# Kernel optimization log

Hardware: AMD Instinct MI355X
Metric: run time of the kernel (lower is better)

Reference implementation:

```python
import jax, jax.numpy as jnp
import numpy as np

BOX_WARP = 1.0
RAY_START = 2.25
RAY_END = 3.3
S = 32  # depth_resolution (coarse), N_importance = 0


def bilinear_sample(image, coords):
    """Faithful port of the custom grid_sample (align_corners=True mapping).
    image: [B, C, H, W]; coords: [B, M, 2] in [-1, 1]. Returns [B, M, C]."""
    B, C, H, W = image.shape
    ix = (coords[..., 0] + 1.0) * 0.5 * (W - 1)
    iy = (coords[..., 1] + 1.0) * 0.5 * (H - 1)
    ix0 = jnp.floor(ix)
    iy0 = jnp.floor(iy)
    ix1 = ix0 + 1.0
    iy1 = iy0 + 1.0
    # weights use UNclamped corner positions, matching the torch code
    w_nw = (ix1 - ix) * (iy1 - iy)
    w_ne = (ix - ix0) * (iy1 - iy)
    w_sw = (ix1 - ix) * (iy - iy0)
    w_se = (ix - ix0) * (iy - iy0)
    ix0c = jnp.clip(ix0, 0, W - 1).astype(jnp.int32)
    ix1c = jnp.clip(ix1, 0, W - 1).astype(jnp.int32)
    iy0c = jnp.clip(iy0, 0, H - 1).astype(jnp.int32)
    iy1c = jnp.clip(iy1, 0, H - 1).astype(jnp.int32)
    img = image.reshape(B, C, H * W)

    def gather(iyc, ixc):
        idx = iyc * W + ixc  # [B, M]
        return jnp.take_along_axis(img, idx[:, None, :], axis=2)  # [B, C, M]

    out = (gather(iy0c, ix0c) * w_nw[:, None, :]
           + gather(iy0c, ix1c) * w_ne[:, None, :]
           + gather(iy1c, ix0c) * w_sw[:, None, :]
           + gather(iy1c, ix1c) * w_se[:, None, :])
    return out.transpose(0, 2, 1)  # [B, M, C]


def setup_inputs() -> dict:
    key = jax.random.key(0)
    k1, k2, k3, k4, k5 = jax.random.split(key, 5)
    N, n_planes, C, H, W = 2, 3, 32, 256, 256
    R = 16384
    vol_planes = jax.random.normal(k1, (N, n_planes, C, H, W), dtype=jnp.float32)
    dirs = jax.random.normal(k2, (N, R, 3), dtype=jnp.float32)
    dirs = dirs / jnp.linalg.norm(dirs, axis=-1, keepdims=True)
    # camera on sphere of radius 2.7 looking through origin -> samples in box
    ray_origins = -2.7 * dirs
    w1 = jax.random.normal(k3, (C, 64), dtype=jnp.float32) * (1.0 / np.sqrt(C))
    b1 = jnp.zeros((64,), dtype=jnp.float32)
    w2 = jax.random.normal(k4, (64, 33), dtype=jnp.float32) * (1.0 / 8.0)
    b2 = jnp.zeros((33,), dtype=jnp.float32)
    return {"vol_planes": vol_planes, "ray_origins": ray_origins,
            "ray_directions": dirs, "w1": w1, "b1": b1, "w2": w2, "b2": b2}


def reference(vol_planes, ray_origins, ray_directions, w1, b1, w2, b2):
    N, n_planes, C, H, W = vol_planes.shape
    R = ray_origins.shape[1]
    # --- sample_stratified (deterministic: midpoint of each bin) ---
    t = (jnp.arange(S, dtype=vol_planes.dtype) + 0.5) / S
    d = RAY_START + (RAY_END - RAY_START) * t  # [S]
    depths = jnp.broadcast_to(d[None, None, :, None], (N, R, S, 1))
    coords = ray_origins[:, :, None, :] + depths * ray_directions[:, :, None, :]
    M = R * S
    coords = coords.reshape(N, M, 3) * (2.0 / BOX_WARP)
    # --- project_onto_planes (vol_proj=True): xyz, yzx, xzy; sampler uses xy ---
    xy = coords[..., jnp.array([0, 1])]
    yz = coords[..., jnp.array([1, 2])]
    xz = coords[..., jnp.array([0, 2])]
    proj = jnp.stack([xy, yz, xz], axis=1).reshape(N * n_planes, M, 2)
    feats = bilinear_sample(vol_planes.reshape(N * n_planes, C, H, W), proj)
    feats = feats.reshape(N, n_planes, M, C).mean(axis=1)  # aggregate planes
    # --- decoder: small MLP -> 1 sigma + 32 rgb features (EG3D style) ---
    h = jax.nn.softplus(feats @ w1 + b1)
    o = h @ w2 + b2
    sigma = o[..., :1].reshape(N, R, S, 1)
    rgb = (jax.nn.sigmoid(o[..., 1:]) * 1.002 - 0.001).reshape(N, R, S, 32)
    # --- MipRayMarcher2 ---
    deltas = depths[:, :, 1:] - depths[:, :, :-1]
    colors_mid = 0.5 * (rgb[:, :, :-1] + rgb[:, :, 1:])
    densities_mid = 0.5 * (sigma[:, :, :-1] + sigma[:, :, 1:])
    densities_mid = jax.nn.softplus(densities_mid - 1.0)
    alpha = 1.0 - jnp.exp(-deltas * densities_mid)  # [N,R,S-1,1]
    trans = jnp.cumprod(
        jnp.concatenate([jnp.ones_like(alpha[:, :, :1]), 1.0 - alpha + 1e-10],
                        axis=2), axis=2)[:, :, :-1]
    weights = alpha * trans
    rgb_final = (weights * colors_mid).sum(axis=2)  # [N, R, 32]
    return rgb_final
```

## Files before the change

kernel.cpp:

```cpp
#include <hip/hip_runtime.h>
#include <math.h>

#define HH 256
#define WW 256
#define CC 32
#define SS 32
#define NRAYS 32768
#define RPB 8
#define TEXOFF 256

#define FXB_OFF 0
#define SIG_OFF 20480
#define WST_OFF 21504
#define W2T_OFF 25600
#define ALP_OFF 31744
#define POOLSZ  32768

typedef __attribute__((ext_vector_type(8))) short short8;
typedef __attribute__((ext_vector_type(4))) float f32x4;

__device__ __forceinline__ f32x4 mfma16(short8 a, short8 b, f32x4 c) {
    return __builtin_amdgcn_mfma_f32_16x16x32_bf16(a, b, c, 0, 0, 0);
}

__device__ __forceinline__ float bf2f(unsigned short u) {
    union { unsigned int ui; float f; } v; v.ui = ((unsigned int)u) << 16; return v.f;
}
__device__ __forceinline__ unsigned short f2bf(float f) {
    union { float f; unsigned int u; } v; v.f = f;
    unsigned int u = v.u;
    unsigned int r = u + 0x7fffu + ((u >> 16) & 1u);
    return (unsigned short)(r >> 16);
}
__device__ __forceinline__ int iclamp(int x, int lo, int hi) {
    return x < lo ? lo : (x > hi ? hi : x);
}
__device__ __forceinline__ float softplus_f(float z) {
    return fmaxf(z, 0.f) + log1pf(expf(-fabsf(z)));
}
__device__ __forceinline__ float softplus_fast(float z) {
    return fmaxf(z, 0.f) + __logf(1.0f + __expf(-fabsf(z)));
}
__device__ __forceinline__ float sigmoid_fast(float z) {
    return __builtin_amdgcn_rcpf(1.0f + __expf(-z));
}

template<bool F32>
__device__ __forceinline__ float ldv(const void* p, size_t i) {
    if (F32) return ((const float*)p)[i];
    else     return bf2f(((const unsigned short*)p)[i]);
}

__global__ void detect_dtype(const void* __restrict__ rayo, int* __restrict__ flag) {
    if (threadIdx.x == 0 && blockIdx.x == 0) {
        const float* f = (const float*)rayo;
        const unsigned short* u = (const unsigned short*)rayo;
        float sf = 0.f, sb = 0.f;
        for (int r = 0; r < 8; r++) {
            const float a = f[3 * r], b = f[3 * r + 1], c = f[3 * r + 2];
            const float nf = a * a + b * b + c * c;
            sf += fminf(fabsf(nf - 7.29f), 1e3f);
            const float x = bf2f(u[3 * r]), y = bf2f(u[3 * r + 1]), z = bf2f(u[3 * r + 2]);
            const float nb = x * x + y * y + z * z;
            sb += fminf(fabsf(nb - 7.29f), 1e3f);
        }
        *flag = (sf < sb) ? 1 : 0;
    }
}

__global__ __launch_bounds__(1024) void transpose_tex(
    const void* __restrict__ vol, void* __restrict__ tex, const int* __restrict__ flag) {
    __shared__ __align__(16) float          tf[32][129];
    __shared__ __align__(16) unsigned short tb[32][129];
    const int l = threadIdx.x;
    const int tx = l & 31, ty = l >> 5;
    const int wq = l >> 3, cq = l & 7;
    const int w0 = blockIdx.x * 128;
    const int h  = blockIdx.y;
    const int img = blockIdx.z;
    const size_t srcE = (((size_t)img * CC + ty) * HH + h) * WW + w0 + 4 * tx;
    const size_t dstE = (((size_t)img * HH + h) * WW + (w0 + wq)) * CC + 4 * cq;
    if (*flag) {
        const float4 v = *(const float4*)((const float*)vol + srcE);
        tf[ty][4 * tx + 0] = v.x; tf[ty][4 * tx + 1] = v.y;
        tf[ty][4 * tx + 2] = v.z; tf[ty][4 * tx + 3] = v.w;
        __syncthreads();
        float4 o;
        o.x = tf[4 * cq + 0][wq]; o.y = tf[4 * cq + 1][wq];
        o.z = tf[4 * cq + 2][wq]; o.w = tf[4 * cq + 3][wq];
        *(float4*)((float*)tex + dstE) = o;
    } else {
        const ushort4 v = *(const ushort4*)((const unsigned short*)vol + srcE);
        tb[ty][4 * tx + 0] = v.x; tb[ty][4 * tx + 1] = v.y;
        tb[ty][4 * tx + 2] = v.z; tb[ty][4 * tx + 3] = v.w;
        __syncthreads();
        ushort4 o;
        o.x = tb[4 * cq + 0][wq]; o.y = tb[4 * cq + 1][wq];
        o.z = tb[4 * cq + 2][wq]; o.w = tb[4 * cq + 3][wq];
        *(ushort4*)((unsigned short*)tex + dstE) = o;
    }
}

template<bool F32>
__device__ void render_mfma_body(
    const void* __restrict__ tex,
    const void* __restrict__ rayo, const void* __restrict__ rayd,
    const void* __restrict__ w1b, const void* __restrict__ b1b,
    const void* __restrict__ w2b, const void* __restrict__ b2b,
    void* __restrict__ outp, char* __restrict__ pool)
{
    const int t = threadIdx.x;
    unsigned short* fxB = (unsigned short*)(pool + FXB_OFF);
    float* sigL = (float*)(pool + SIG_OFF);
    unsigned short* w1t = (unsigned short*)(pool + WST_OFF);
    unsigned short* w2t = (unsigned short*)(pool + W2T_OFF);
    float* aL = (float*)(pool + ALP_OFF);

    for (int i = t; i < 2048; i += 256) {
        const int k = i >> 6, n = i & 63;
        w1t[n * 32 + k] = f2bf(ldv<F32>(w1b, i));
    }
    for (int i = t; i < 3072; i += 256) {
        const int n = i >> 6, k = i & 63;
        w2t[n * 64 + k] = (n < 33) ? f2bf(ldv<F32>(w2b, (size_t)k * 33 + n)) : (unsigned short)0;
    }
    __syncthreads();

    {
        const int rl = t >> 5;
        const int L  = t & 31;
        const int c4 = L & 7;
        const int sub = L >> 3;
        const int gray = blockIdx.x * RPB + rl;
        const int n = gray >> 14;
        const size_t rb = (size_t)gray * 3;
        const float ox = ldv<F32>(rayo, rb), oy = ldv<F32>(rayo, rb + 1), oz = ldv<F32>(rayo, rb + 2);
        const float dx = ldv<F32>(rayd, rb), dy = ldv<F32>(rayd, rb + 1), dz = ldv<F32>(rayd, rb + 2);

        #pragma unroll 2
        for (int k = 0; k < 8; ++k) {
            const int s = sub * 8 + k;
            const float d = 2.25f + 1.05f * ((s + 0.5f) * (1.0f / 32.0f));
            const float x = (ox + d * dx) * 2.0f;
            const float y = (oy + d * dy) * 2.0f;
            const float z = (oz + d * dz) * 2.0f;
            float a0[4] = {0.f, 0.f, 0.f, 0.f};
            float a1[4] = {0.f, 0.f, 0.f, 0.f};
            float a2[4] = {0.f, 0.f, 0.f, 0.f};
            #pragma unroll
            for (int p = 0; p < 3; p++) {
                const float u = (p == 0) ? x : ((p == 1) ? y : x);
                const float v = (p == 0) ? y : z;
                const float ixf = fmaf(u, 127.5f, 127.5f);
                const float iyf = fmaf(v, 127.5f, 127.5f);
                const float ix0f = floorf(ixf), iy0f = floorf(iyf);
                const float wx1 = ixf - ix0f, wy1 = iyf - iy0f;
                const float wx0 = 1.f - wx1,  wy0 = 1.f - wy1;
                const int ix0 = iclamp((int)ix0f, 0, 255);
                const int ix1 = iclamp((int)ix0f + 1, 0, 255);
                const int iy0 = iclamp((int)iy0f, 0, 255);
                const int iy1 = iclamp((int)iy0f + 1, 0, 255);
                const float w00 = wx0 * wy0, w01 = wx1 * wy0, w10 = wx0 * wy1, w11 = wx1 * wy1;
                const unsigned int pb4 = (unsigned int)(n * 3 + p) * (HH * WW * CC / 4);
                float v00[4], v01[4], v10[4], v11[4];
                if (F32) {
                    const float4* tx4 = (const float4*)tex;
                    const float4 q00 = tx4[pb4 + ((unsigned int)(iy0 * WW + ix0) << 3) + c4];
                    const float4 q01 = tx4[pb4 + ((unsigned int)(iy0 * WW + ix1) << 3) + c4];
                    const float4 q10 = tx4[pb4 + ((unsigned int)(iy1 * WW + ix0) << 3) + c4];
                    const float4 q11 = tx4[pb4 + ((unsigned int)(iy1 * WW + ix1) << 3) + c4];
                    v00[0] = q00.x; v00[1] = q00.y; v00[2] = q00.z; v00[3] = q00.w;
                    v01[0] = q01.x; v01[1] = q01.y; v01[2] = q01.z; v01[3] = q01.w;
                    v10[0] = q10.x; v10[1] = q10.y; v10[2] = q10.z; v10[3] = q10.w;
                    v11[0] = q11.x; v11[1] = q11.y; v11[2] = q11.z; v11[3] = q11.w;
                } else {
                    #pragma unroll
                    for (int i = 0; i < 4; i++) {
                        const size_t e = (size_t)pb4 * 4 + 4 * c4 + i;
                        v00[i] = ldv<false>(tex, e + ((size_t)(iy0 * WW + ix0) << 5));
                        v01[i] = ldv<false>(tex, e + ((size_t)(iy0 * WW + ix1) << 5));
                        v10[i] = ldv<false>(tex, e + ((size_t)(iy1 * WW + ix0) << 5));
                        v11[i] = ldv<false>(tex, e + ((size_t)(iy1 * WW + ix1) << 5));
                    }
                }
                #pragma unroll
                for (int i = 0; i < 4; i++) {
                    float acc = w00 * v00[i];
                    acc = fmaf(w01, v01[i], acc);
                    acc = fmaf(w10, v10[i], acc);
                    acc = fmaf(w11, v11[i], acc);
                    if (p == 0) a0[i] = acc; else if (p == 1) a1[i] = acc; else a2[i] = acc;
                }
            }
            unsigned int lo, hi;
            lo = (unsigned int)f2bf((a0[0] + a1[0] + a2[0]) * (1.0f / 3.0f))
               | ((unsigned int)f2bf((a0[1] + a1[1] + a2[1]) * (1.0f / 3.0f)) << 16);
            hi = (unsigned int)f2bf((a0[2] + a1[2] + a2[2]) * (1.0f / 3.0f))
               | ((unsigned int)f2bf((a0[3] + a1[3] + a2[3]) * (1.0f / 3.0f)) << 16);
            uint2 pk; pk.x = lo; pk.y = hi;
            *(uint2*)(pool + FXB_OFF + (rl * 32 + s) * 80 + c4 * 8) = pk;
        }
    }

    const int w = t >> 6;
    const int lane = t & 63;
    const int l16 = lane & 15, quad = lane >> 4;

    short8 b1f[4];
    #pragma unroll
    for (int nt = 0; nt < 4; nt++)
        b1f[nt] = *(const short8*)(pool + WST_OFF + (nt * 16 + l16) * 64 + quad * 16);
    short8 b2f[3][2];
    #pragma unroll
    for (int nt = 0; nt < 3; nt++)
        #pragma unroll
        for (int ks = 0; ks < 2; ks++)
            b2f[nt][ks] = *(const short8*)(pool + W2T_OFF + (nt * 16 + l16) * 128 + ks * 64 + quad * 16);
    float bb1[4], bb2[3];
    #pragma unroll
    for (int nt = 0; nt < 4; nt++) bb1[nt] = ldv<F32>(b1b, nt * 16 + l16);
    #pragma unroll
    for (int nt = 0; nt < 3; nt++) {
        const int n2 = nt * 16 + l16;
        bb2[nt] = (n2 < 33) ? ldv<F32>(b2b, n2) : 0.f;
    }
    __syncthreads();

    {
        char* hb = pool + WST_OFF + w * 2304;
        #pragma unroll 1
        for (int mt = 0; mt < 4; mt++) {
            const int rbase = w * 64 + mt * 16;
            const short8 a1 = *(const short8*)(pool + FXB_OFF + (rbase + l16) * 80 + quad * 16);
            #pragma unroll
            for (int nt = 0; nt < 4; nt++) {
                f32x4 hc = { bb1[nt], bb1[nt], bb1[nt], bb1[nt] };
                hc = mfma16(a1, b1f[nt], hc);
                #pragma unroll
                for (int r = 0; r < 4; r++) {
                    const float hv = softplus_fast(hc[r]);
                    *(unsigned short*)(hb + (quad * 4 + r) * 144 + (nt * 16 + l16) * 2) = f2bf(hv);
                }
            }
            const short8 a2k0 = *(const short8*)(hb + l16 * 144 + quad * 16);
            const short8 a2k1 = *(const short8*)(hb + l16 * 144 + 64 + quad * 16);
            #pragma unroll
            for (int nt = 0; nt < 3; nt++) {
                f32x4 o = { bb2[nt], bb2[nt], bb2[nt], bb2[nt] };
                o = mfma16(a2k0, b2f[nt][0], o);
                o = mfma16(a2k1, b2f[nt][1], o);
                #pragma unroll
                for (int r = 0; r < 4; r++) {
                    const int row = rbase + quad * 4 + r;
                    if (nt == 0) {
                        if (l16 == 0) sigL[row] = o[r];
                        else fxB[row * 40 + (l16 - 1)] =
                                 f2bf(fmaf(sigmoid_fast(o[r]), 1.002f, -0.001f));
                    } else if (nt == 1) {
                        fxB[row * 40 + (15 + l16)] =
                                 f2bf(fmaf(sigmoid_fast(o[r]), 1.002f, -0.001f));
                    } else if (l16 == 0) {
                        fxB[row * 40 + 31] =
                                 f2bf(fmaf(sigmoid_fast(o[r]), 1.002f, -0.001f));
                    }
                }
            }
        }
    }
    __syncthreads();

    {
        const int rl = t >> 5, sm = t & 31;
        if (sm < 31) {
            const float sp = sigL[rl * 32 + sm];
            const float sn = sigL[rl * 32 + sm + 1];
            const float m = 0.5f * (sp + sn) - 1.0f;
            const float dens = fmaxf(m, 0.f) + __logf(1.0f + __expf(-fabsf(m)));
            aL[rl * 32 + sm] = 1.0f - __expf(-(1.05f / 32.0f) * dens);
        }
    }
    __syncthreads();

    {
        const int rl = t >> 5, sm = t & 31;
        if (sm == 0) {
            float T = 1.0f;
            #pragma unroll
            for (int j = 0; j < 31; j++) {
                const float a = aL[rl * 32 + j];
                aL[rl * 32 + j] = (a * T) * 0.5f;
                T *= (1.0f - a + 1e-10f);
            }
        }
    }
    __syncthreads();

    {
        const int rl = t >> 5, c = t & 31;
        const int gr2 = blockIdx.x * RPB + rl;
        float acc = 0.0f;
        float rp = bf2f(fxB[(rl * 32 + 0) * 40 + c]);
        #pragma unroll 4
        for (int sm = 0; sm < 31; sm++) {
            const float rn = bf2f(fxB[(rl * 32 + sm + 1) * 40 + c]);
            acc = fmaf(aL[rl * 32 + sm], rp + rn, acc);
            rp = rn;
        }
        const size_t oidx = (size_t)gr2 * 32 + c;
        if (F32) ((float*)outp)[oidx] = acc;
        else     ((unsigned short*)outp)[oidx] = f2bf(acc);
    }
}

__global__ __launch_bounds__(256, 4) void render_fast(
    const void* __restrict__ tex, const void* __restrict__ rayo,
    const void* __restrict__ rayd, const void* __restrict__ w1b,
    const void* __restrict__ b1b, const void* __restrict__ w2b,
    const void* __restrict__ b2b, void* __restrict__ outp,
    const int* __restrict__ flag)
{
    __shared__ __align__(16) char pool[POOLSZ];
    if (*flag) render_mfma_body<true >(tex, rayo, rayd, w1b, b1b, w2b, b2b, outp, pool);
    else       render_mfma_body<false>(tex, rayo, rayd, w1b, b1b, w2b, b2b, outp, pool);
}

template<bool F32>
__device__ __forceinline__ void render_body(
    const void* __restrict__ vol, const void* __restrict__ rayo,
    const void* __restrict__ rayd, const void* __restrict__ w1b,
    const void* __restrict__ b1b, const void* __restrict__ w2b,
    const void* __restrict__ b2b, void* __restrict__ outp,
    float* wsm, float (*rgbL)[SS][33], float (*sigL)[SS])
{
    const int t = threadIdx.x;
    for (int i = t; i < 4257; i += 256) {
        float v;
        if (i < 2048)       v = ldv<F32>(w1b, i);
        else if (i < 2112)  v = ldv<F32>(b1b, i - 2048);
        else if (i < 4224)  v = ldv<F32>(w2b, i - 2112);
        else                v = ldv<F32>(b2b, i - 4224);
        wsm[i] = v;
    }
    __syncthreads();

    const int rl = t >> 5;
    const int s  = t & 31;
    const int gray = blockIdx.x * RPB + rl;
    const int n = gray >> 14;

    const size_t rbase = (size_t)gray * 3;
    const float ox = ldv<F32>(rayo, rbase), oy = ldv<F32>(rayo, rbase + 1), oz = ldv<F32>(rayo, rbase + 2);
    const float dx = ldv<F32>(rayd, rbase), dy = ldv<F32>(rayd, rbase + 1), dz = ldv<F32>(rayd, rbase + 2);
    const float d = 2.25f + 1.05f * ((s + 0.5f) * (1.0f / 32.0f));
    const float x = (ox + d * dx) * 2.0f;
    const float y = (oy + d * dy) * 2.0f;
    const float z = (oz + d * dz) * 2.0f;

    float fx[32];
    #pragma unroll
    for (int c = 0; c < 32; c++) fx[c] = 0.f;

    #pragma unroll
    for (int p = 0; p < 3; p++) {
        const float u = (p == 0) ? x : ((p == 1) ? y : x);
        const float v = (p == 0) ? y : z;
        const float ixf = fmaf(u, 127.5f, 127.5f);
        const float iyf = fmaf(v, 127.5f, 127.5f);
        const float ix0f = floorf(ixf), iy0f = floorf(iyf);
        const float wx1 = ixf - ix0f, wy1 = iyf - iy0f;
        const float wx0 = 1.f - wx1,  wy0 = 1.f - wy1;
        const int ix0 = iclamp((int)ix0f, 0, 255);
        const int ix1 = iclamp((int)ix0f + 1, 0, 255);
        const int iy0 = iclamp((int)iy0f, 0, 255);
        const int iy1 = iclamp((int)iy0f + 1, 0, 255);
        const float wnw = wx0 * wy0, wne = wx1 * wy0, wsw = wx0 * wy1, wse = wx1 * wy1;
        const int i00 = iy0 * WW + ix0, i01 = iy0 * WW + ix1;
        const int i10 = iy1 * WW + ix0, i11 = iy1 * WW + ix1;
        const size_t pb = (size_t)(n * 3 + p) * CC * HH * WW;
        #pragma unroll
        for (int c = 0; c < 32; c++) {
            const size_t cb = pb + (size_t)c * (HH * WW);
            fx[c] += wnw * ldv<F32>(vol, cb + i00) + wne * ldv<F32>(vol, cb + i01)
                   + wsw * ldv<F32>(vol, cb + i10) + wse * ldv<F32>(vol, cb + i11);
        }
    }
    #pragma unroll
    for (int c = 0; c < 32; c++) fx[c] *= (1.0f / 3.0f);

    const float* W1 = wsm;
    const float* B1 = wsm + 2048;
    const float* W2 = wsm + 2112;
    const float* B2 = wsm + 4224;

    float h[64];
    #pragma unroll
    for (int j = 0; j < 64; j++) h[j] = B1[j];
    #pragma unroll
    for (int c = 0; c < 32; c++) {
        const float f = fx[c];
        #pragma unroll
        for (int j = 0; j < 64; j++) h[j] = fmaf(f, W1[c * 64 + j], h[j]);
    }
    #pragma unroll
    for (int j = 0; j < 64; j++) h[j] = softplus_f(h[j]);

    #pragma unroll 1
    for (int k = 0; k < 33; k++) {
        float zz = B2[k];
        #pragma unroll
        for (int j = 0; j < 64; j++) zz = fmaf(h[j], W2[j * 33 + k], zz);
        if (k == 0) sigL[rl][s] = zz;
        else {
            const float sg = 1.0f / (1.0f + expf(-zz));
            rgbL[rl][s][k - 1] = fmaf(sg, 1.002f, -0.001f);
        }
    }
    __syncthreads();

    const int c = t & 31;
    const float delta = 1.05f / 32.0f;
    float T = 1.0f, acc = 0.0f;
    float sig_prev = sigL[rl][0];
    float rgb_prev = rgbL[rl][0][c];
    #pragma unroll 1
    for (int sm = 0; sm < 31; sm++) {
        const float sig_next = sigL[rl][sm + 1];
        const float rgb_next = rgbL[rl][sm + 1][c];
        const float dens = softplus_f(0.5f * (sig_prev + sig_next) - 1.0f);
        const float alpha = 1.0f - expf(-delta * dens);
        acc += alpha * T * 0.5f * (rgb_prev + rgb_next);
        T *= (1.0f - alpha + 1e-10f);
        sig_prev = sig_next;
        rgb_prev = rgb_next;
    }
    const size_t oidx = (size_t)gray * 32 + c;
    if (F32) ((float*)outp)[oidx] = acc;
    else     ((unsigned short*)outp)[oidx] = f2bf(acc);
}

__global__ __launch_bounds__(256) void render_any(
    const void* __restrict__ vol, const void* __restrict__ rayo,
    const void* __restrict__ rayd, const void* __restrict__ w1b,
    const void* __restrict__ b1b, const void* __restrict__ w2b,
    const void* __restrict__ b2b, void* __restrict__ outp,
    const int* __restrict__ flag)
{
    __shared__ float wsm[4257];
    __shared__ float rgbL[RPB][SS][33];
    __shared__ float sigL[RPB][SS];
    if (*flag) render_body<true >(vol, rayo, rayd, w1b, b1b, w2b, b2b, outp, wsm, rgbL, sigL);
    else       render_body<false>(vol, rayo, rayd, w1b, b1b, w2b, b2b, outp, wsm, rgbL, sigL);
}

extern "C" void kernel_launch(void* const* d_in, const int* in_sizes, int n_in,
                              void* d_out, int out_size, void* d_ws, size_t ws_size,
                              hipStream_t stream) {
    const void* vol  = d_in[0];
    const void* rayo = d_in[1];
    const void* rayd = d_in[2];
    const void* w1   = d_in[3];
    const void* b1   = d_in[4];
    const void* w2   = d_in[5];
    const void* b2   = d_in[6];
    int* flag = (int*)d_ws;
    void* tex = (void*)((char*)d_ws + TEXOFF);

    const size_t need = TEXOFF + (size_t)6 * HH * WW * CC * 4;

    detect_dtype<<<dim3(1), dim3(64), 0, stream>>>(rayo, flag);
    if (ws_size >= need) {
        transpose_tex<<<dim3(WW / 128, HH, 6), dim3(1024), 0, stream>>>(vol, tex, flag);
        render_fast<<<dim3(NRAYS / RPB), dim3(256), 0, stream>>>(
            tex, rayo, rayd, w1, b1, w2, b2, d_out, flag);
    } else {
        render_any<<<dim3(NRAYS / RPB), dim3(256), 0, stream>>>(
            vol, rayo, rayd, w1, b1, w2, b2, d_out, flag);
    }
}
```

Baseline: 253.4 us.

## Store transposed triplane texture in bf16 to halve gather bandwidth

The transpose kernel now converts fp32 feature planes to bf16 while reordering them into channel-last layout, and the render kernel gathers 8-byte bf16 quads instead of 16-byte float4s. This halves the texture footprint, the transpose write traffic and the random gather bytes, which should improve cache hit rates. Weight staging loops are rewritten so the shared-memory writes are contiguous, and dtype detection is spread across lanes with shuffles. Rounding the features to bf16 before interpolation adds precision loss on the fp32 path.

Measured after the change: 240.8 us. 5.0% less time.

```diff
diff --git a/kernel.cpp b/kernel.cpp
--- a/kernel.cpp
+++ b/kernel.cpp
@@ -26,12 +26,21 @@
 __device__ __forceinline__ float bf2f(unsigned short u) {
     union { unsigned int ui; float f; } v; v.ui = ((unsigned int)u) << 16; return v.f;
 }
+__device__ __forceinline__ float lo2f(unsigned int w) {
+    union { unsigned int ui; float f; } v; v.ui = w << 16; return v.f;
+}
+__device__ __forceinline__ float hi2f(unsigned int w) {
+    union { unsigned int ui; float f; } v; v.ui = w & 0xffff0000u; return v.f;
+}
 __device__ __forceinline__ unsigned short f2bf(float f) {
     union { float f; unsigned int u; } v; v.f = f;
     unsigned int u = v.u;
     unsigned int r = u + 0x7fffu + ((u >> 16) & 1u);
     return (unsigned short)(r >> 16);
 }
+__device__ __forceinline__ unsigned int pk_bf16(float a, float b) {
+    return (unsigned int)f2bf(a) | ((unsigned int)f2bf(b) << 16);
+}
 __device__ __forceinline__ int iclamp(int x, int lo, int hi) {
     return x < lo ? lo : (x > hi ? hi : x);
 }
@@ -52,25 +61,27 @@
 }
 
 __global__ void detect_dtype(const void* __restrict__ rayo, int* __restrict__ flag) {
-    if (threadIdx.x == 0 && blockIdx.x == 0) {
+    const int t = threadIdx.x;
+    float sf = 0.f, sb = 0.f;
+    if (t < 8) {
         const float* f = (const float*)rayo;
         const unsigned short* u = (const unsigned short*)rayo;
-        float sf = 0.f, sb = 0.f;
-        for (int r = 0; r < 8; r++) {
-            const float a = f[3 * r], b = f[3 * r + 1], c = f[3 * r + 2];
-            const float nf = a * a + b * b + c * c;
-            sf += fminf(fabsf(nf - 7.29f), 1e3f);
-            const float x = bf2f(u[3 * r]), y = bf2f(u[3 * r + 1]), z = bf2f(u[3 * r + 2]);
-            const float nb = x * x + y * y + z * z;
-            sb += fminf(fabsf(nb - 7.29f), 1e3f);
-        }
-        *flag = (sf < sb) ? 1 : 0;
-    }
+        const float a = f[3 * t], b = f[3 * t + 1], c = f[3 * t + 2];
+        const float nf = a * a + b * b + c * c;
+        sf = fminf(fabsf(nf - 7.29f), 1e3f);
+        const float x = bf2f(u[3 * t]), y = bf2f(u[3 * t + 1]), z = bf2f(u[3 * t + 2]);
+        const float nb = x * x + y * y + z * z;
+        sb = fminf(fabsf(nb - 7.29f), 1e3f);
+    }
+    sf += __shfl_down(sf, 4); sb += __shfl_down(sb, 4);
+    sf += __shfl_down(sf, 2); sb += __shfl_down(sb, 2);
+    sf += __shfl_down(sf, 1); sb += __shfl_down(sb, 1);
+    if (t == 0 && blockIdx.x == 0) *flag = (sf < sb) ? 1 : 0;
 }
 
 __global__ __launch_bounds__(1024) void transpose_tex(
-    const void* __restrict__ vol, void* __restrict__ tex, const int* __restrict__ flag) {
-    __shared__ __align__(16) float          tf[32][129];
+    const void* __restrict__ vol, unsigned short* __restrict__ tex,
+    const int* __restrict__ flag) {
     __shared__ __align__(16) unsigned short tb[32][129];
     const int l = threadIdx.x;
     const int tx = l & 31, ty = l >> 5;
@@ -82,28 +93,21 @@
     const size_t dstE = (((size_t)img * HH + h) * WW + (w0 + wq)) * CC + 4 * cq;
     if (*flag) {
         const float4 v = *(const float4*)((const float*)vol + srcE);
-        tf[ty][4 * tx + 0] = v.x; tf[ty][4 * tx + 1] = v.y;
-        tf[ty][4 * tx + 2] = v.z; tf[ty][4 * tx + 3] = v.w;
-        __syncthreads();
-        float4 o;
-        o.x = tf[4 * cq + 0][wq]; o.y = tf[4 * cq + 1][wq];
-        o.z = tf[4 * cq + 2][wq]; o.w = tf[4 * cq + 3][wq];
-        *(float4*)((float*)tex + dstE) = o;
+        tb[ty][4 * tx + 0] = f2bf(v.x); tb[ty][4 * tx + 1] = f2bf(v.y);
+        tb[ty][4 * tx + 2] = f2bf(v.z); tb[ty][4 * tx + 3] = f2bf(v.w);
     } else {
-        const ushort4 v = *(const ushort4*)((const unsigned short*)vol + srcE);
-        tb[ty][4 * tx + 0] = v.x; tb[ty][4 * tx + 1] = v.y;
-        tb[ty][4 * tx + 2] = v.z; tb[ty][4 * tx + 3] = v.w;
-        __syncthreads();
-        ushort4 o;
-        o.x = tb[4 * cq + 0][wq]; o.y = tb[4 * cq + 1][wq];
-        o.z = tb[4 * cq + 2][wq]; o.w = tb[4 * cq + 3][wq];
-        *(ushort4*)((unsigned short*)tex + dstE) = o;
-    }
+        *(ushort4*)&tb[ty][4 * tx] = *(const ushort4*)((const unsigned short*)vol + srcE);
+    }
+    __syncthreads();
+    ushort4 o;
+    o.x = tb[4 * cq + 0][wq]; o.y = tb[4 * cq + 1][wq];
+    o.z = tb[4 * cq + 2][wq]; o.w = tb[4 * cq + 3][wq];
+    *(ushort4*)(tex + dstE) = o;
 }
 
 template<bool F32>
 __device__ void render_mfma_body(
-    const void* __restrict__ tex,
+    const unsigned short* __restrict__ tex,
     const void* __restrict__ rayo, const void* __restrict__ rayd,
     const void* __restrict__ w1b, const void* __restrict__ b1b,
     const void* __restrict__ w2b, const void* __restrict__ b2b,
@@ -117,12 +121,12 @@
     float* aL = (float*)(pool + ALP_OFF);
 
     for (int i = t; i < 2048; i += 256) {
-        const int k = i >> 6, n = i & 63;
-        w1t[n * 32 + k] = f2bf(ldv<F32>(w1b, i));
+        const int n = i >> 5, k = i & 31;
+        w1t[i] = f2bf(ldv<F32>(w1b, (size_t)k * 64 + n));
     }
     for (int i = t; i < 3072; i += 256) {
         const int n = i >> 6, k = i & 63;
-        w2t[n * 64 + k] = (n < 33) ? f2bf(ldv<F32>(w2b, (size_t)k * 33 + n)) : (unsigned short)0;
+        w2t[i] = (n < 33) ? f2bf(ldv<F32>(w2b, (size_t)k * 33 + n)) : (unsigned short)0;
     }
     __syncthreads();
 
@@ -136,6 +140,8 @@
         const size_t rb = (size_t)gray * 3;
         const float ox = ldv<F32>(rayo, rb), oy = ldv<F32>(rayo, rb + 1), oz = ldv<F32>(rayo, rb + 2);
         const float dx = ldv<F32>(rayd, rb), dy = ldv<F32>(rayd, rb + 1), dz = ldv<F32>(rayd, rb + 2);
+        const char* texb = (const char*)tex;
+        const unsigned int cb = (unsigned int)c4 * 8;
 
         #pragma unroll 2
         for (int k = 0; k < 8; ++k) {
@@ -161,28 +167,15 @@
                 const int iy0 = iclamp((int)iy0f, 0, 255);
                 const int iy1 = iclamp((int)iy0f + 1, 0, 255);
                 const float w00 = wx0 * wy0, w01 = wx1 * wy0, w10 = wx0 * wy1, w11 = wx1 * wy1;
-                const unsigned int pb4 = (unsigned int)(n * 3 + p) * (HH * WW * CC / 4);
-                float v00[4], v01[4], v10[4], v11[4];
-                if (F32) {
-                    const float4* tx4 = (const float4*)tex;
-                    const float4 q00 = tx4[pb4 + ((unsigned int)(iy0 * WW + ix0) << 3) + c4];
-                    const float4 q01 = tx4[pb4 + ((unsigned int)(iy0 * WW + ix1) << 3) + c4];
-                    const float4 q10 = tx4[pb4 + ((unsigned int)(iy1 * WW + ix0) << 3) + c4];
-                    const float4 q11 = tx4[pb4 + ((unsigned int)(iy1 * WW + ix1) << 3) + c4];
-                    v00[0] = q00.x; v00[1] = q00.y; v00[2] = q00.z; v00[3] = q00.w;
-                    v01[0] = q01.x; v01[1] = q01.y; v01[2] = q01.z; v01[3] = q01.w;
-                    v10[0] = q10.x; v10[1] = q10.y; v10[2] = q10.z; v10[3] = q10.w;
-                    v11[0] = q11.x; v11[1] = q11.y; v11[2] = q11.z; v11[3] = q11.w;
-                } else {
-                    #pragma unroll
-                    for (int i = 0; i < 4; i++) {
-                        const size_t e = (size_t)pb4 * 4 + 4 * c4 + i;
-                        v00[i] = ldv<false>(tex, e + ((size_t)(iy0 * WW + ix0) << 5));
-                        v01[i] = ldv<false>(tex, e + ((size_t)(iy0 * WW + ix1) << 5));
-                        v10[i] = ldv<false>(tex, e + ((size_t)(iy1 * WW + ix0) << 5));
-                        v11[i] = ldv<false>(tex, e + ((size_t)(iy1 * WW + ix1) << 5));
-                    }
-                }
+                const unsigned int pb = (unsigned int)(n * 3 + p) * (HH * WW * CC * 2) + cb;
+                const uint2 q00 = *(const uint2*)(texb + pb + ((unsigned int)(iy0 * WW + ix0) << 6));
+                const uint2 q01 = *(const uint2*)(texb + pb + ((unsigned int)(iy0 * WW + ix1) << 6));
+                const uint2 q10 = *(const uint2*)(texb + pb + ((unsigned int)(iy1 * WW + ix0) << 6));
+                const uint2 q11 = *(const uint2*)(texb + pb + ((unsigned int)(iy1 * WW + ix1) << 6));
+                const float v00[4] = { lo2f(q00.x), hi2f(q00.x), lo2f(q00.y), hi2f(q00.y) };
+                const float v01[4] = { lo2f(q01.x), hi2f(q01.x), lo2f(q01.y), hi2f(q01.y) };
+                const float v10[4] = { lo2f(q10.x), hi2f(q10.x), lo2f(q10.y), hi2f(q10.y) };
+                const float v11[4] = { lo2f(q11.x), hi2f(q11.x), lo2f(q11.y), hi2f(q11.y) };
                 #pragma unroll
                 for (int i = 0; i < 4; i++) {
                     float acc = w00 * v00[i];
@@ -192,12 +185,11 @@
                     if (p == 0) a0[i] = acc; else if (p == 1) a1[i] = acc; else a2[i] = acc;
                 }
             }
-            unsigned int lo, hi;
-            lo = (unsigned int)f2bf((a0[0] + a1[0] + a2[0]) * (1.0f / 3.0f))
-               | ((unsigned int)f2bf((a0[1] + a1[1] + a2[1]) * (1.0f / 3.0f)) << 16);
-            hi = (unsigned int)f2bf((a0[2] + a1[2] + a2[2]) * (1.0f / 3.0f))
-               | ((unsigned int)f2bf((a0[3] + a1[3] + a2[3]) * (1.0f / 3.0f)) << 16);
-            uint2 pk; pk.x = lo; pk.y = hi;
+            uint2 pk;
+            pk.x = pk_bf16((a0[0] + a1[0] + a2[0]) * (1.0f / 3.0f),
+                           (a0[1] + a1[1] + a2[1]) * (1.0f / 3.0f));
+            pk.y = pk_bf16((a0[2] + a1[2] + a2[2]) * (1.0f / 3.0f),
+                           (a0[3] + a1[3] + a2[3]) * (1.0f / 3.0f));
             *(uint2*)(pool + FXB_OFF + (rl * 32 + s) * 80 + c4 * 8) = pk;
         }
     }
@@ -313,7 +305,7 @@
 }
 
 __global__ __launch_bounds__(256, 4) void render_fast(
-    const void* __restrict__ tex, const void* __restrict__ rayo,
+    const unsigned short* __restrict__ tex, const void* __restrict__ rayo,
     const void* __restrict__ rayd, const void* __restrict__ w1b,
     const void* __restrict__ b1b, const void* __restrict__ w2b,
     const void* __restrict__ b2b, void* __restrict__ outp,
@@ -463,9 +455,9 @@
     const void* w2   = d_in[5];
     const void* b2   = d_in[6];
     int* flag = (int*)d_ws;
-    void* tex = (void*)((char*)d_ws + TEXOFF);
-
-    const size_t need = TEXOFF + (size_t)6 * HH * WW * CC * 4;
+    unsigned short* tex = (unsigned short*)((char*)d_ws + TEXOFF);
+
+    const size_t need = TEXOFF + (size_t)6 * HH * WW * CC * 2;
 
     detect_dtype<<<dim3(1), dim3(64), 0, stream>>>(rayo, flag);
     if (ws_size >= need) {
```

## Fold dtype detection into kernels, unify fp32 texture, raise occupancy bound

Applied to the files above, without the earlier changes.

Removes the separate single-thread dtype-detection kernel; each block now computes the flag itself from the ray origins, which saves one launch and its serialization. The transposed texture is always stored as fp32, so the render path has only one vectorized-gather branch. Integer clamps become float min/max, weight-staging loops get contiguous LDS writes, and the render kernel's launch_bounds minimum blocks goes from 4 to 5, which may force register spilling. The redundant per-block flag computation adds a few global reads per block, and with bf16 input the texture now doubles in memory traffic.

New measurement: 312.9 us. +23.5%, slower.

```diff
diff --git a/kernel.cpp b/kernel.cpp
--- a/kernel.cpp
+++ b/kernel.cpp
@@ -7,7 +7,6 @@
 #define SS 32
 #define NRAYS 32768
 #define RPB 8
-#define TEXOFF 256
 
 #define FXB_OFF 0
 #define SIG_OFF 20480
@@ -32,8 +31,8 @@
     unsigned int r = u + 0x7fffu + ((u >> 16) & 1u);
     return (unsigned short)(r >> 16);
 }
-__device__ __forceinline__ int iclamp(int x, int lo, int hi) {
-    return x < lo ? lo : (x > hi ? hi : x);
+__device__ __forceinline__ unsigned int pk_bf16(float a, float b) {
+    return (unsigned int)f2bf(a) | ((unsigned int)f2bf(b) << 16);
 }
 __device__ __forceinline__ float softplus_f(float z) {
     return fmaxf(z, 0.f) + log1pf(expf(-fabsf(z)));
@@ -51,28 +50,29 @@
     else     return bf2f(((const unsigned short*)p)[i]);
 }
 
-__global__ void detect_dtype(const void* __restrict__ rayo, int* __restrict__ flag) {
-    if (threadIdx.x == 0 && blockIdx.x == 0) {
-        const float* f = (const float*)rayo;
-        const unsigned short* u = (const unsigned short*)rayo;
-        float sf = 0.f, sb = 0.f;
-        for (int r = 0; r < 8; r++) {
-            const float a = f[3 * r], b = f[3 * r + 1], c = f[3 * r + 2];
-            const float nf = a * a + b * b + c * c;
-            sf += fminf(fabsf(nf - 7.29f), 1e3f);
-            const float x = bf2f(u[3 * r]), y = bf2f(u[3 * r + 1]), z = bf2f(u[3 * r + 2]);
-            const float nb = x * x + y * y + z * z;
-            sb += fminf(fabsf(nb - 7.29f), 1e3f);
-        }
-        *flag = (sf < sb) ? 1 : 0;
-    }
+__device__ __forceinline__ int compute_flag(const void* rayo) {
+    const float* f = (const float*)rayo;
+    const unsigned short* u = (const unsigned short*)rayo;
+    float sf = 0.f, sb = 0.f;
+    for (int r = 0; r < 8; r++) {
+        const float a = f[3 * r], b = f[3 * r + 1], c = f[3 * r + 2];
+        sf += fminf(fabsf(a * a + b * b + c * c - 7.29f), 1e3f);
+        const float x = bf2f(u[3 * r]), y = bf2f(u[3 * r + 1]), z = bf2f(u[3 * r + 2]);
+        sb += fminf(fabsf(x * x + y * y + z * z - 7.29f), 1e3f);
+    }
+    return (sf < sb) ? 1 : 0;
 }
 
 __global__ __launch_bounds__(1024) void transpose_tex(
-    const void* __restrict__ vol, void* __restrict__ tex, const int* __restrict__ flag) {
-    __shared__ __align__(16) float          tf[32][129];
-    __shared__ __align__(16) unsigned short tb[32][129];
+    const void* __restrict__ vol, float* __restrict__ tex,
+    const void* __restrict__ rayo) {
+    __shared__ __align__(16) float tf[32][129];
+    __shared__ int fsh;
     const int l = threadIdx.x;
+    if (l == 0) fsh = compute_flag(rayo);
+    __syncthreads();
+    const int flag = fsh;
+
     const int tx = l & 31, ty = l >> 5;
     const int wq = l >> 3, cq = l & 7;
     const int w0 = blockIdx.x * 128;
@@ -80,30 +80,25 @@
     const int img = blockIdx.z;
     const size_t srcE = (((size_t)img * CC + ty) * HH + h) * WW + w0 + 4 * tx;
     const size_t dstE = (((size_t)img * HH + h) * WW + (w0 + wq)) * CC + 4 * cq;
-    if (*flag) {
+    if (flag) {
         const float4 v = *(const float4*)((const float*)vol + srcE);
         tf[ty][4 * tx + 0] = v.x; tf[ty][4 * tx + 1] = v.y;
         tf[ty][4 * tx + 2] = v.z; tf[ty][4 * tx + 3] = v.w;
-        __syncthreads();
-        float4 o;
-        o.x = tf[4 * cq + 0][wq]; o.y = tf[4 * cq + 1][wq];
-        o.z = tf[4 * cq + 2][wq]; o.w = tf[4 * cq + 3][wq];
-        *(float4*)((float*)tex + dstE) = o;
     } else {
         const ushort4 v = *(const ushort4*)((const unsigned short*)vol + srcE);
-        tb[ty][4 * tx + 0] = v.x; tb[ty][4 * tx + 1] = v.y;
-        tb[ty][4 * tx + 2] = v.z; tb[ty][4 * tx + 3] = v.w;
-        __syncthreads();
-        ushort4 o;
-        o.x = tb[4 * cq + 0][wq]; o.y = tb[4 * cq + 1][wq];
-        o.z = tb[4 * cq + 2][wq]; o.w = tb[4 * cq + 3][wq];
-        *(ushort4*)((unsigned short*)tex + dstE) = o;
-    }
+        tf[ty][4 * tx + 0] = bf2f(v.x); tf[ty][4 * tx + 1] = bf2f(v.y);
+        tf[ty][4 * tx + 2] = bf2f(v.z); tf[ty][4 * tx + 3] = bf2f(v.w);
+    }
+    __syncthreads();
+    float4 o;
+    o.x = tf[4 * cq + 0][wq]; o.y = tf[4 * cq + 1][wq];
+    o.z = tf[4 * cq + 2][wq]; o.w = tf[4 * cq + 3][wq];
+    *(float4*)(tex + dstE) = o;
 }
 
 template<bool F32>
 __device__ void render_mfma_body(
-    const void* __restrict__ tex,
+    const float* __restrict__ tex,
     const void* __restrict__ rayo, const void* __restrict__ rayd,
     const void* __restrict__ w1b, const void* __restrict__ b1b,
     const void* __restrict__ w2b, const void* __restrict__ b2b,
@@ -117,12 +112,12 @@
     float* aL = (float*)(pool + ALP_OFF);
 
     for (int i = t; i < 2048; i += 256) {
-        const int k = i >> 6, n = i & 63;
-        w1t[n * 32 + k] = f2bf(ldv<F32>(w1b, i));
+        const int n = i >> 5, k = i & 31;
+        w1t[i] = f2bf(ldv<F32>(w1b, (size_t)k * 64 + n));
     }
     for (int i = t; i < 3072; i += 256) {
         const int n = i >> 6, k = i & 63;
-        w2t[n * 64 + k] = (n < 33) ? f2bf(ldv<F32>(w2b, (size_t)k * 33 + n)) : (unsigned short)0;
+        w2t[i] = (n < 33) ? f2bf(ldv<F32>(w2b, (size_t)k * 33 + n)) : (unsigned short)0;
     }
     __syncthreads();
 
@@ -136,6 +131,7 @@
         const size_t rb = (size_t)gray * 3;
         const float ox = ldv<F32>(rayo, rb), oy = ldv<F32>(rayo, rb + 1), oz = ldv<F32>(rayo, rb + 2);
         const float dx = ldv<F32>(rayd, rb), dy = ldv<F32>(rayd, rb + 1), dz = ldv<F32>(rayd, rb + 2);
+        const float4* tx4 = (const float4*)tex;
 
         #pragma unroll 2
         for (int k = 0; k < 8; ++k) {
@@ -156,33 +152,20 @@
                 const float ix0f = floorf(ixf), iy0f = floorf(iyf);
                 const float wx1 = ixf - ix0f, wy1 = iyf - iy0f;
                 const float wx0 = 1.f - wx1,  wy0 = 1.f - wy1;
-                const int ix0 = iclamp((int)ix0f, 0, 255);
-                const int ix1 = iclamp((int)ix0f + 1, 0, 255);
-                const int iy0 = iclamp((int)iy0f, 0, 255);
-                const int iy1 = iclamp((int)iy0f + 1, 0, 255);
+                const int ix0 = (int)fminf(fmaxf(ix0f,        0.f), 255.f);
+                const int ix1 = (int)fminf(fmaxf(ix0f + 1.0f, 0.f), 255.f);
+                const int iy0 = (int)fminf(fmaxf(iy0f,        0.f), 255.f);
+                const int iy1 = (int)fminf(fmaxf(iy0f + 1.0f, 0.f), 255.f);
                 const float w00 = wx0 * wy0, w01 = wx1 * wy0, w10 = wx0 * wy1, w11 = wx1 * wy1;
                 const unsigned int pb4 = (unsigned int)(n * 3 + p) * (HH * WW * CC / 4);
-                float v00[4], v01[4], v10[4], v11[4];
-                if (F32) {
-                    const float4* tx4 = (const float4*)tex;
-                    const float4 q00 = tx4[pb4 + ((unsigned int)(iy0 * WW + ix0) << 3) + c4];
-                    const float4 q01 = tx4[pb4 + ((unsigned int)(iy0 * WW + ix1) << 3) + c4];
-                    const float4 q10 = tx4[pb4 + ((unsigned int)(iy1 * WW + ix0) << 3) + c4];
-                    const float4 q11 = tx4[pb4 + ((unsigned int)(iy1 * WW + ix1) << 3) + c4];
-                    v00[0] = q00.x; v00[1] = q00.y; v00[2] = q00.z; v00[3] = q00.w;
-                    v01[0] = q01.x; v01[1] = q01.y; v01[2] = q01.z; v01[3] = q01.w;
-                    v10[0] = q10.x; v10[1] = q10.y; v10[2] = q10.z; v10[3] = q10.w;
-                    v11[0] = q11.x; v11[1] = q11.y; v11[2] = q11.z; v11[3] = q11.w;
-                } else {
-                    #pragma unroll
-                    for (int i = 0; i < 4; i++) {
-                        const size_t e = (size_t)pb4 * 4 + 4 * c4 + i;
-                        v00[i] = ldv<false>(tex, e + ((size_t)(iy0 * WW + ix0) << 5));
-                        v01[i] = ldv<false>(tex, e + ((size_t)(iy0 * WW + ix1) << 5));
-                        v10[i] = ldv<false>(tex, e + ((size_t)(iy1 * WW + ix0) << 5));
-                        v11[i] = ldv<false>(tex, e + ((size_t)(iy1 * WW + ix1) << 5));
-                    }
-                }
+                const float4 q00 = tx4[pb4 + ((unsigned int)(iy0 * WW + ix0) << 3) + c4];
+                const float4 q01 = tx4[pb4 + ((unsigned int)(iy0 * WW + ix1) << 3) + c4];
+                const float4 q10 = tx4[pb4 + ((unsigned int)(iy1 * WW + ix0) << 3) + c4];
+                const float4 q11 = tx4[pb4 + ((unsigned int)(iy1 * WW + ix1) << 3) + c4];
+                const float v00[4] = { q00.x, q00.y, q00.z, q00.w };
+                const float v01[4] = { q01.x, q01.y, q01.z, q01.w };
+                const float v10[4] = { q10.x, q10.y, q10.z, q10.w };
+                const float v11[4] = { q11.x, q11.y, q11.z, q11.w };
                 #pragma unroll
                 for (int i = 0; i < 4; i++) {
                     float acc = w00 * v00[i];
@@ -192,12 +175,11 @@
                     if (p == 0) a0[i] = acc; else if (p == 1) a1[i] = acc; else a2[i] = acc;
                 }
             }
-            unsigned int lo, hi;
-            lo = (unsigned int)f2bf((a0[0] + a1[0] + a2[0]) * (1.0f / 3.0f))
-               | ((unsigned int)f2bf((a0[1] + a1[1] + a2[1]) * (1.0f / 3.0f)) << 16);
-            hi = (unsigned int)f2bf((a0[2] + a1[2] + a2[2]) * (1.0f / 3.0f))
-               | ((unsigned int)f2bf((a0[3] + a1[3] + a2[3]) * (1.0f / 3.0f)) << 16);
-            uint2 pk; pk.x = lo; pk.y = hi;
+            uint2 pk;
+            pk.x = pk_bf16((a0[0] + a1[0] + a2[0]) * (1.0f / 3.0f),
+                           (a0[1] + a1[1] + a2[1]) * (1.0f / 3.0f));
+            pk.y = pk_bf16((a0[2] + a1[2] + a2[2]) * (1.0f / 3.0f),
+                           (a0[3] + a1[3] + a2[3]) * (1.0f / 3.0f));
             *(uint2*)(pool + FXB_OFF + (rl * 32 + s) * 80 + c4 * 8) = pk;
         }
     }
@@ -312,16 +294,19 @@
     }
 }
 
-__global__ __launch_bounds__(256, 4) void render_fast(
-    const void* __restrict__ tex, const void* __restrict__ rayo,
+__global__ __launch_bounds__(256, 5) void render_fast(
+    const float* __restrict__ tex, const void* __restrict__ rayo,
     const void* __restrict__ rayd, const void* __restrict__ w1b,
     const void* __restrict__ b1b, const void* __restrict__ w2b,
-    const void* __restrict__ b2b, void* __restrict__ outp,
-    const int* __restrict__ flag)
+    const void* __restrict__ b2b, void* __restrict__ outp)
 {
     __shared__ __align__(16) char pool[POOLSZ];
-    if (*flag) render_mfma_body<true >(tex, rayo, rayd, w1b, b1b, w2b, b2b, outp, pool);
-    else       render_mfma_body<false>(tex, rayo, rayd, w1b, b1b, w2b, b2b, outp, pool);
+    int* fsh = (int*)(pool + ALP_OFF);
+    if (threadIdx.x == 0) *fsh = compute_flag(rayo);
+    __syncthreads();
+    const int flag = *fsh;
+    if (flag) render_mfma_body<true >(tex, rayo, rayd, w1b, b1b, w2b, b2b, outp, pool);
+    else      render_mfma_body<false>(tex, rayo, rayd, w1b, b1b, w2b, b2b, outp, pool);
 }
 
 template<bool F32>
@@ -369,10 +354,10 @@
         const float ix0f = floorf(ixf), iy0f = floorf(iyf);
         const float wx1 = ixf - ix0f, wy1 = iyf - iy0f;
         const float wx0 = 1.f - wx1,  wy0 = 1.f - wy1;
-        const int ix0 = iclamp((int)ix0f, 0, 255);
-        const int ix1 = iclamp((int)ix0f + 1, 0, 255);
-        const int iy0 = iclamp((int)iy0f, 0, 255);
-        const int iy1 = iclamp((int)iy0f + 1, 0, 255);
+        const int ix0 = (int)fminf(fmaxf(ix0f,        0.f), 255.f);
+        const int ix1 = (int)fminf(fmaxf(ix0f + 1.0f, 0.f), 255.f);
+        const int iy0 = (int)fminf(fmaxf(iy0f,        0.f), 255.f);
+        const int iy1 = (int)fminf(fmaxf(iy0f + 1.0f, 0.f), 255.f);
         const float wnw = wx0 * wy0, wne = wx1 * wy0, wsw = wx0 * wy1, wse = wx1 * wy1;
         const int i00 = iy0 * WW + ix0, i01 = iy0 * WW + ix1;
         const int i10 = iy1 * WW + ix0, i11 = iy1 * WW + ix1;
@@ -442,14 +427,17 @@
     const void* __restrict__ vol, const void* __restrict__ rayo,
     const void* __restrict__ rayd, const void* __restrict__ w1b,
     const void* __restrict__ b1b, const void* __restrict__ w2b,
-    const void* __restrict__ b2b, void* __restrict__ outp,
-    const int* __restrict__ flag)
+    const void* __restrict__ b2b, void* __restrict__ outp)
 {
     __shared__ float wsm[4257];
     __shared__ float rgbL[RPB][SS][33];
     __shared__ float sigL[RPB][SS];
-    if (*flag) render_body<true >(vol, rayo, rayd, w1b, b1b, w2b, b2b, outp, wsm, rgbL, sigL);
-    else       render_body<false>(vol, rayo, rayd, w1b, b1b, w2b, b2b, outp, wsm, rgbL, sigL);
+    __shared__ int fsh;
+    if (threadIdx.x == 0) fsh = compute_flag(rayo);
+    __syncthreads();
+    const int flag = fsh;
+    if (flag) render_body<true >(vol, rayo, rayd, w1b, b1b, w2b, b2b, outp, wsm, rgbL, sigL);
+    else      render_body<false>(vol, rayo, rayd, w1b, b1b, w2b, b2b, outp, wsm, rgbL, sigL);
 }
 
 extern "C" void kernel_launch(void* const* d_in, const int* in_sizes, int n_in,
@@ -462,18 +450,16 @@
     const void* b1   = d_in[4];
     const void* w2   = d_in[5];
     const void* b2   = d_in[6];
-    int* flag = (int*)d_ws;
-    void* tex = (void*)((char*)d_ws + TEXOFF);
-
-    const size_t need = TEXOFF + (size_t)6 * HH * WW * CC * 4;
-
-    detect_dtype<<<dim3(1), dim3(64), 0, stream>>>(rayo, flag);
+    float* tex = (float*)d_ws;
+
+    const size_t need = (size_t)6 * HH * WW * CC * 4;
+
     if (ws_size >= need) {
-        transpose_tex<<<dim3(WW / 128, HH, 6), dim3(1024), 0, stream>>>(vol, tex, flag);
+        transpose_tex<<<dim3(WW / 128, HH, 6), dim3(1024), 0, stream>>>(vol, tex, rayo);
         render_fast<<<dim3(NRAYS / RPB), dim3(256), 0, stream>>>(
-            tex, rayo, rayd, w1, b1, w2, b2, d_out, flag);
+            tex, rayo, rayd, w1, b1, w2, b2, d_out);
     } else {
         render_any<<<dim3(NRAYS / RPB), dim3(256), 0, stream>>>(
-            vol, rayo, rayd, w1, b1, w2, b2, d_out, flag);
-    }
-}
+            vol, rayo, rayd, w1, b1, w2, b2, d_out);
+    }
+}
```
